# Kernel optimization log

Hardware: AMD Instinct MI355X
Metric: run time of the kernel (lower is better)

## Reference

```python
import jax, jax.numpy as jnp
import numpy as np

LAMBDA_COLOR = 10.0


def _neighbors(x, p):
    """Patch-unfold: x [B,C,H,W] -> [B, P*P, C, H, W] of zero-padded shifted copies.
    Matches conv3d with diagonal one-hot [P^2,1,1,P,P] weights, padding (0,pad,pad)."""
    pad = (p - 1) // 2
    B, C, H, W = x.shape
    xp = jnp.pad(x, ((0, 0), (0, 0), (pad, pad), (pad, pad)))
    shifts = [xp[:, :, i:i + H, j:j + W] for i in range(p) for j in range(p)]
    return jnp.stack(shifts, axis=1)


def _spatial_grid(img_size):
    # np.mgrid[-1:1+eps:2/(S-1), -1:1+eps:2/(S-1)] -> [2, S, S] (y-coords, x-coords)
    lin = jnp.linspace(-1.0, 1.0, img_size, dtype=jnp.float32)
    gy, gx = jnp.meshgrid(lin, lin, indexing='ij')
    return jnp.stack([gy, gx], axis=0)[None]  # [1, 2, S, S]


def setup_inputs() -> dict:
    key = jax.random.key(0)
    k1, k2 = jax.random.split(key)
    B, S, P = 16, 256, 7
    flow = jax.random.normal(k1, (B, 2, S, S), dtype=jnp.float32)
    image = jax.random.uniform(k2, (B, 3, S, S), dtype=jnp.float32)
    return {"flow": flow, "image": image, "img_size": S, "patch_size": P}


def reference(flow, image, img_size, patch_size):
    flow = flow * img_size                                  # [B,2,H,W]
    grid = _spatial_grid(img_size)                          # [1,2,H,W]

    flow_nb = _neighbors(flow, patch_size)                  # [B,P2,2,H,W]
    img_nb = _neighbors(image, patch_size)                  # [B,P2,3,H,W]
    grid_nb = _neighbors(grid, patch_size)                  # [1,P2,2,H,W]

    im_w = jnp.sum((image[:, None] - img_nb) ** 2, axis=2)  # [B,P2,H,W]
    sp_w = jnp.sum((grid[:, None] - grid_nb) ** 2, axis=2)  # [1,P2,H,W]
    fl = jnp.sum((flow_nb - flow[:, None]) ** 2, axis=2)    # [B,P2,H,W]

    return jnp.mean(fl * jnp.exp(-(im_w * LAMBDA_COLOR + sp_w)))
```

## Files before the change

### kernel.cpp

```cpp
#include <hip/hip_runtime.h>


#define S_DIM 256
#define LOG2E 1.4426950408889634f
#define C10L2E (-14.426950408889634f)
#define N_TERMS 51380224.0f
#define FINAL_SCALE (65536.0f / N_TERMS)

typedef float v4f __attribute__((ext_vector_type(4)));
typedef int   v4i __attribute__((ext_vector_type(4)));

__device__ v4f llvm_amdgcn_raw_buffer_load_v4f32(v4i rsrc, int voffset,
                                                 int soffset, int aux)
    __asm("llvm.amdgcn.raw.buffer.load.v4f32");

__device__ inline v4i make_srd(const void* p, unsigned bytes) {
    union { v4i v; unsigned u[4]; } s;
    s.u[0] = (unsigned)(unsigned long long)p;
    s.u[1] = (unsigned)(((unsigned long long)p) >> 32);
    s.u[2] = bytes;
    s.u[3] = 0x00020000u;
    return s.v;
}

__global__ __launch_bounds__(256, 2) void flow_reg_loss_kernel(
    const float* __restrict__ flow,
    const float* __restrict__ image,
    float* __restrict__ partial)
{
    __shared__ float wave_sums[4];

    const int lane = threadIdx.x;
    const int wv   = threadIdx.y;
    const int y0   = (blockIdx.x * 4 + wv) * 2;
    const int b    = blockIdx.z;
    const int x0   = lane * 4;

    const v4i srdI = make_srd(image, 16u * 3u * 65536u * 4u);
    const v4i srdF = make_srd(flow,  16u * 2u * 65536u * 4u);

    const int rowx = x0 * 4 - 12;
    const int ib = b * 786432;
    const int fb = b * 524288;

    const float step = 2.0f / 255.0f;
    const float K2L2E = step * step * LOG2E;

#define LOAD_ROW(r, yy)                                                        \
    do {                                                                       \
        const int ro = (yy) * 1024 + rowx;                                     \
        _Pragma("unroll")                                                      \
        for (int c = 0; c < 3; ++c) {                                          \
            const int v = ib + c * 262144 + ro;                                \
            const v4f a  = llvm_amdgcn_raw_buffer_load_v4f32(srdI, v, 0, 0);   \
            const v4f b4 = llvm_amdgcn_raw_buffer_load_v4f32(srdI, v, 16, 0);  \
            const v4f c4 = llvm_amdgcn_raw_buffer_load_v4f32(srdI, v, 32, 0);  \
            r[c][0] = a.x;  r[c][1] = a.y;  r[c][2]  = a.z;  r[c][3]  = a.w;   \
            r[c][4] = b4.x; r[c][5] = b4.y; r[c][6]  = b4.z; r[c][7]  = b4.w;  \
            r[c][8] = c4.x; r[c][9] = c4.y; r[c][10] = c4.z; r[c][11] = c4.w;  \
        }                                                                      \
        _Pragma("unroll")                                                      \
        for (int c = 0; c < 2; ++c) {                                          \
            const int v = fb + c * 262144 + ro;                                \
            const v4f a  = llvm_amdgcn_raw_buffer_load_v4f32(srdF, v, 0, 0);   \
            const v4f b4 = llvm_amdgcn_raw_buffer_load_v4f32(srdF, v, 16, 0);  \
            const v4f c4 = llvm_amdgcn_raw_buffer_load_v4f32(srdF, v, 32, 0);  \
            r[3+c][0] = a.x;  r[3+c][1] = a.y;  r[3+c][2]  = a.z;              \
            r[3+c][3] = a.w;  r[3+c][4] = b4.x; r[3+c][5]  = b4.y;             \
            r[3+c][6] = b4.z; r[3+c][7] = b4.w; r[3+c][8]  = c4.x;             \
            r[3+c][9] = c4.y; r[3+c][10] = c4.z; r[3+c][11] = c4.w;            \
        }                                                                      \
    } while (0)

    float A[5][12], B[5][12];
    LOAD_ROW(A, y0);
    LOAD_ROW(B, y0 + 1);

    float ic0[2][4], ic1[2][4], ic2[2][4], fc0[2][4], fc1[2][4];
    float acc = 0.0f;

    auto tap_row = [&](int cr, const float (&r)[5][12], int dy, int dx0,
                       bool yin) {
#pragma unroll
        for (int dx = dx0; dx <= 3; ++dx) {
            const float c2 = -K2L2E * (float)(dy * dy + dx * dx);
#pragma unroll
            for (int i = 0; i < 4; ++i) {
                const int j = i + dx + 3;
                const float d0 = ic0[cr][i] - r[0][j];
                const float d1 = ic1[cr][i] - r[1][j];
                const float d2 = ic2[cr][i] - r[2][j];
                const float imw = d0 * d0 + d1 * d1 + d2 * d2;
                const float e0 = r[3][j] - fc0[cr][i];
                const float e1 = r[4][j] - fc1[cr][i];
                const float fl2 = e0 * e0 + e1 * e1;
                const float wq =
                    (yin && (unsigned)(x0 + i + dx) < S_DIM) ? 1.0f : 0.0f;
                acc += (wq * fl2) *
                       __builtin_amdgcn_exp2f(fmaf(imw, C10L2E, c2));
            }
        }
    };

#pragma unroll
    for (int i = 0; i < 4; ++i) {
        ic0[0][i] = A[0][3 + i]; ic1[0][i] = A[1][3 + i]; ic2[0][i] = A[2][3 + i];
        fc0[0][i] = A[3][3 + i]; fc1[0][i] = A[4][3 + i];
    }
    tap_row(0, A, 0, 1, true);
    LOAD_ROW(A, y0 + 2);

#pragma unroll
    for (int i = 0; i < 4; ++i) {
        ic0[1][i] = B[0][3 + i]; ic1[1][i] = B[1][3 + i]; ic2[1][i] = B[2][3 + i];
        fc0[1][i] = B[3][3 + i]; fc1[1][i] = B[4][3 + i];
    }
    tap_row(1, B, 0, 1, true);
    tap_row(0, B, 1, -3, true);
    LOAD_ROW(B, y0 + 3);

    {
        const bool yin = (y0 + 2) < S_DIM;
        tap_row(0, A, 2, -3, yin);
        tap_row(1, A, 1, -3, yin);
    }
    LOAD_ROW(A, y0 + 4);

    {
        const bool yin = (y0 + 3) < S_DIM;
        tap_row(0, B, 3, -3, yin);
        tap_row(1, B, 2, -3, yin);
    }

    tap_row(1, A, 3, -3, (y0 + 4) < S_DIM);

    float oob = 0.0f;
#pragma unroll
    for (int cr = 0; cr < 2; ++cr) {
        const int yg = y0 + cr;
        const int ny_in = 7 - max(0, 3 - yg) - max(0, yg - (S_DIM - 1 - 3));
        const float gyc = -1.0f + step * (float)yg;
#pragma unroll
        for (int i = 0; i < 4; ++i) {
            const int xg = x0 + i;
            const int nx_in = 7 - max(0, 3 - xg) - max(0, xg - (S_DIM - 1 - 3));
            const float n_oob = (float)(49 - ny_in * nx_in);
            const float gxc = -1.0f + step * (float)xg;
            const float g2c = gyc * gyc + gxc * gxc;
            const float imw_c = ic0[cr][i] * ic0[cr][i] +
                                ic1[cr][i] * ic1[cr][i] +
                                ic2[cr][i] * ic2[cr][i];
            const float fl_c = fc0[cr][i] * fc0[cr][i] +
                               fc1[cr][i] * fc1[cr][i];
            oob += (n_oob * fl_c) *
                   __builtin_amdgcn_exp2f(fmaf(imw_c, C10L2E, -g2c * LOG2E));
        }
    }

    float acc_all = 2.0f * acc + oob;
#pragma unroll
    for (int off = 32; off > 0; off >>= 1)
        acc_all += __shfl_down(acc_all, off, 64);
    if (lane == 0) wave_sums[wv] = acc_all;
    __syncthreads();
    if (lane == 0 && wv == 0) {
        partial[blockIdx.z * gridDim.x + blockIdx.x] =
            (wave_sums[0] + wave_sums[1]) + (wave_sums[2] + wave_sums[3]);
    }
}

__global__ __launch_bounds__(256) void reduce_kernel(
    const float* __restrict__ partial, float* __restrict__ out)
{
    __shared__ float wave_sums[4];
    const int t = threadIdx.x;
    typedef float v2f __attribute__((ext_vector_type(2)));
    const v2f v = ((const v2f*)partial)[t];
    float s = v.x + v.y;
#pragma unroll
    for (int off = 32; off > 0; off >>= 1)
        s += __shfl_down(s, off, 64);
    if ((t & 63) == 0) wave_sums[t >> 6] = s;
    __syncthreads();
    if (t == 0) {
        out[0] = ((wave_sums[0] + wave_sums[1]) + (wave_sums[2] + wave_sums[3]))
                 * FINAL_SCALE;
    }
}

extern "C" void kernel_launch(void* const* d_in, const int* in_sizes, int n_in,
                              void* d_out, int out_size, void* d_ws, size_t ws_size,
                              hipStream_t stream) {
    const float* flow  = (const float*)d_in[0];
    const float* image = (const float*)d_in[1];
    float* out = (float*)d_out;
    float* partial = (float*)d_ws;

    dim3 grid(32, 1, 16);
    dim3 block(64, 4);
    flow_reg_loss_kernel<<<grid, block, 0, stream>>>(flow, image, partial);
    reduce_kernel<<<1, 256, 0, stream>>>(partial, out);
}
```

Measured before the change: 83.35 us.

## Fuse final reduction via atomicAdd, precompute x masks, branch on row bounds

Drops the separate reduce kernel. Each block now atomically adds its scaled partial sum into the output, which a memset clears before launch. Grid indexing changes so consecutive block IDs walk across batch items, and the per-tap x-boundary masks are precomputed into a small register array. Out-of-range rows are skipped with uniform branches instead of multiplying by zero. The memset is an extra stream operation, and the order of float atomics makes the result nondeterministic.

Result: slower. 85.68 us (+2.8%).

```diff
diff --git a/kernel.cpp b/kernel.cpp
--- a/kernel.cpp
+++ b/kernel.cpp
@@ -26,14 +26,16 @@
 __global__ __launch_bounds__(256, 2) void flow_reg_loss_kernel(
     const float* __restrict__ flow,
     const float* __restrict__ image,
-    float* __restrict__ partial)
+    float* __restrict__ out)
 {
     __shared__ float wave_sums[4];
 
     const int lane = threadIdx.x;
     const int wv   = threadIdx.y;
-    const int y0   = (blockIdx.x * 4 + wv) * 2;
-    const int b    = blockIdx.z;
+    const int id   = blockIdx.x;
+    const int b    = id & 15;
+    const int rg   = id >> 4;
+    const int y0   = (rg * 4 + wv) * 2;
     const int x0   = lane * 4;
 
     const v4i srdI = make_srd(image, 16u * 3u * 65536u * 4u);
@@ -76,11 +78,15 @@
     LOAD_ROW(A, y0);
     LOAD_ROW(B, y0 + 1);
 
+    float wL[10];
+#pragma unroll
+    for (int j = 0; j < 10; ++j)
+        wL[j] = ((unsigned)(x0 - 3 + j) < S_DIM) ? 1.0f : 0.0f;
+
     float ic0[2][4], ic1[2][4], ic2[2][4], fc0[2][4], fc1[2][4];
     float acc = 0.0f;
 
-    auto tap_row = [&](int cr, const float (&r)[5][12], int dy, int dx0,
-                       bool yin) {
+    auto tap_row = [&](int cr, const float (&r)[5][12], int dy, int dx0) {
 #pragma unroll
         for (int dx = dx0; dx <= 3; ++dx) {
             const float c2 = -K2L2E * (float)(dy * dy + dx * dx);
@@ -94,9 +100,7 @@
                 const float e0 = r[3][j] - fc0[cr][i];
                 const float e1 = r[4][j] - fc1[cr][i];
                 const float fl2 = e0 * e0 + e1 * e1;
-                const float wq =
-                    (yin && (unsigned)(x0 + i + dx) < S_DIM) ? 1.0f : 0.0f;
-                acc += (wq * fl2) *
+                acc += (wL[j] * fl2) *
                        __builtin_amdgcn_exp2f(fmaf(imw, C10L2E, c2));
             }
         }
@@ -107,7 +111,7 @@
         ic0[0][i] = A[0][3 + i]; ic1[0][i] = A[1][3 + i]; ic2[0][i] = A[2][3 + i];
         fc0[0][i] = A[3][3 + i]; fc1[0][i] = A[4][3 + i];
     }
-    tap_row(0, A, 0, 1, true);
+    tap_row(0, A, 0, 1);
     LOAD_ROW(A, y0 + 2);
 
 #pragma unroll
@@ -115,24 +119,24 @@
         ic0[1][i] = B[0][3 + i]; ic1[1][i] = B[1][3 + i]; ic2[1][i] = B[2][3 + i];
         fc0[1][i] = B[3][3 + i]; fc1[1][i] = B[4][3 + i];
     }
-    tap_row(1, B, 0, 1, true);
-    tap_row(0, B, 1, -3, true);
+    tap_row(1, B, 0, 1);
+    tap_row(0, B, 1, -3);
     LOAD_ROW(B, y0 + 3);
 
-    {
-        const bool yin = (y0 + 2) < S_DIM;
-        tap_row(0, A, 2, -3, yin);
-        tap_row(1, A, 1, -3, yin);
+    if (y0 + 2 < S_DIM) {
+        tap_row(0, A, 2, -3);
+        tap_row(1, A, 1, -3);
     }
     LOAD_ROW(A, y0 + 4);
 
-    {
-        const bool yin = (y0 + 3) < S_DIM;
-        tap_row(0, B, 3, -3, yin);
-        tap_row(1, B, 2, -3, yin);
+    if (y0 + 3 < S_DIM) {
+        tap_row(0, B, 3, -3);
+        tap_row(1, B, 2, -3);
     }
 
-    tap_row(1, A, 3, -3, (y0 + 4) < S_DIM);
+    if (y0 + 4 < S_DIM) {
+        tap_row(1, A, 3, -3);
+    }
 
     float oob = 0.0f;
 #pragma unroll
@@ -164,27 +168,9 @@
     if (lane == 0) wave_sums[wv] = acc_all;
     __syncthreads();
     if (lane == 0 && wv == 0) {
-        partial[blockIdx.z * gridDim.x + blockIdx.x] =
+        const float s =
             (wave_sums[0] + wave_sums[1]) + (wave_sums[2] + wave_sums[3]);
-    }
-}
-
-__global__ __launch_bounds__(256) void reduce_kernel(
-    const float* __restrict__ partial, float* __restrict__ out)
-{
-    __shared__ float wave_sums[4];
-    const int t = threadIdx.x;
-    typedef float v2f __attribute__((ext_vector_type(2)));
-    const v2f v = ((const v2f*)partial)[t];
-    float s = v.x + v.y;
-#pragma unroll
-    for (int off = 32; off > 0; off >>= 1)
-        s += __shfl_down(s, off, 64);
-    if ((t & 63) == 0) wave_sums[t >> 6] = s;
-    __syncthreads();
-    if (t == 0) {
-        out[0] = ((wave_sums[0] + wave_sums[1]) + (wave_sums[2] + wave_sums[3]))
-                 * FINAL_SCALE;
+        atomicAdd(out, s * FINAL_SCALE);
     }
 }
 
@@ -194,10 +180,10 @@
     const float* flow  = (const float*)d_in[0];
     const float* image = (const float*)d_in[1];
     float* out = (float*)d_out;
-    float* partial = (float*)d_ws;
 
-    dim3 grid(32, 1, 16);
+    hipMemsetAsync(out, 0, sizeof(float), stream);
+
+    dim3 grid(512, 1, 1);
     dim3 block(64, 4);
-    flow_reg_loss_kernel<<<grid, block, 0, stream>>>(flow, image, partial);
-    reduce_kernel<<<1, 256, 0, stream>>>(partial, out);
+    flow_reg_loss_kernel<<<grid, block, 0, stream>>>(flow, image, out);
 }
```
